# Optimization experiments

Hardware: AMD Instinct MI355X
Metric: run time of the kernel (lower is better)

## Reference

```python
import jax, jax.numpy as jnp
import numpy as np


def _sobel_kernels():
    # Three 3x3x3 stencils, one per axis: plane at index 0 = -1, plane at index 2 = +1
    # (the torch code also sets kernel[1,1,1]=0, which is already zero).
    ks = []
    for axis in range(3):
        k = np.zeros((3, 3, 3), np.float32)
        sl = [slice(None)] * 3
        sl[axis] = 0
        k[tuple(sl)] = -1.0
        sl[axis] = 2
        k[tuple(sl)] = 1.0
        ks.append(k)
    return np.stack(ks)  # [3, 3, 3, 3]


def setup_inputs() -> dict:
    key = jax.random.key(0)
    x = jax.random.normal(key, (2, 2, 160, 160, 160), dtype=jnp.float32)
    return {"x": x}


def reference(x):
    B, C, D, H, W = x.shape
    # replicate padding (torch F.pad mode='replicate' == jnp 'edge')
    xp = jnp.pad(x, ((0, 0), (0, 0), (1, 1), (1, 1), (1, 1)), mode="edge")
    kernels = jnp.asarray(_sobel_kernels())  # [3,3,3,3]
    # One fused depthwise conv: for each input channel, 3 directional outputs.
    # Grouped conv with feature_group_count=C: output channels [c*3 + d].
    w = jnp.broadcast_to(kernels[None], (C, 3, 3, 3, 3)).reshape(C * 3, 1, 3, 3, 3)
    g = jax.lax.conv_general_dilated(
        xp, w, window_strides=(1, 1, 1), padding="VALID",
        dimension_numbers=("NCDHW", "OIDHW", "NCDHW"),
        feature_group_count=C,
    )  # [B, C*3, D, H, W]
    g = g.reshape(B, C, 3, D, H, W)
    mag = jnp.sqrt(jnp.sum(g * g, axis=2))  # [B, C, D, H, W]
    # torch code cats per-(b,c) [1,1,D,H,W] slices along dim=1 -> [1, B*C, D, H, W]
    return mag.reshape(1, B * C, D, H, W)
```

## Files before the change

kernel.cpp:

```cpp
#include <hip/hip_runtime.h>
#include <math.h>

#define BCn 4
#define Dn 160
#define Hn 160
#define Wn 160
#define HWn (Hn * Wn)
#define W4q (Wn / 4)
#define COLS (Hn * W4q)
#define DCHUNK 5
#define NZC (Dn / DCHUNK)
#define XBLK (COLS / 256)
#define NWR (NZC * BCn)
#define BLOCK 256

typedef float f32x4 __attribute__((ext_vector_type(4)));

struct Plane {
  float4 Rs, Rd, Cs;
};

__device__ __forceinline__ Plane load_plane(const float* __restrict__ xb, int zz,
                                            int rm, int r0, int rp, int w4,
                                            bool ql, bool qr, bool fixL, bool fixR) {
  const int zc = zz < 0 ? 0 : (zz > Dn - 1 ? Dn - 1 : zz);
  const float* p = xb + (size_t)zc * HWn;

  const float4 vm = *(const float4*)(p + rm + w4);
  const float4 v0 = *(const float4*)(p + r0 + w4);
  const float4 vp = *(const float4*)(p + rp + w4);

  float lA = __shfl_up(vm.w, 1);
  float lB = __shfl_up(v0.w, 1);
  float lC = __shfl_up(vp.w, 1);
  float rA = __shfl_down(vm.x, 1);
  float rB = __shfl_down(v0.x, 1);
  float rC = __shfl_down(vp.x, 1);

  if (fixL) {
    lA = p[rm + w4 - 1];
    lB = p[r0 + w4 - 1];
    lC = p[rp + w4 - 1];
  }
  if (fixR) {
    rA = p[rm + w4 + 4];
    rB = p[r0 + w4 + 4];
    rC = p[rp + w4 + 4];
  }

  const float m0 = ql ? vm.x : lA;
  const float c0 = ql ? v0.x : lB;
  const float q0 = ql ? vp.x : lC;
  const float m5 = qr ? vm.w : rA;
  const float c5 = qr ? v0.w : rB;
  const float q5 = qr ? vp.w : rC;

  const float s0 = m0 + c0 + q0;
  const float s1 = vm.x + v0.x + vp.x;
  const float s2 = vm.y + v0.y + vp.y;
  const float s3 = vm.z + v0.z + vp.z;
  const float s4 = vm.w + v0.w + vp.w;
  const float s5 = m5 + c5 + q5;
  const float d0 = q0 - m0;
  const float d1 = vp.x - vm.x;
  const float d2 = vp.y - vm.y;
  const float d3 = vp.z - vm.z;
  const float d4 = vp.w - vm.w;
  const float d5 = q5 - m5;

  Plane out;
  const float t12 = s1 + s2, t23 = s2 + s3, t34 = s3 + s4;
  out.Rs.x = s0 + t12;
  out.Rs.y = t12 + s3;
  out.Rs.z = t23 + s4;
  out.Rs.w = t34 + s5;
  const float u12 = d1 + d2, u23 = d2 + d3, u34 = d3 + d4;
  out.Rd.x = d0 + u12;
  out.Rd.y = u12 + d3;
  out.Rd.z = u23 + d4;
  out.Rd.w = u34 + d5;
  out.Cs.x = s2 - s0;
  out.Cs.y = s3 - s1;
  out.Cs.z = s4 - s2;
  out.Cs.w = s5 - s3;
  return out;
}

__device__ __forceinline__ f32x4 mag4(const Plane& P0, const Plane& P1,
                                      const Plane& P2) {
  const float gdx = P2.Rs.x - P0.Rs.x;
  const float gdy = P2.Rs.y - P0.Rs.y;
  const float gdz = P2.Rs.z - P0.Rs.z;
  const float gdw = P2.Rs.w - P0.Rs.w;
  const float ghx = P0.Rd.x + P1.Rd.x + P2.Rd.x;
  const float ghy = P0.Rd.y + P1.Rd.y + P2.Rd.y;
  const float ghz = P0.Rd.z + P1.Rd.z + P2.Rd.z;
  const float ghw = P0.Rd.w + P1.Rd.w + P2.Rd.w;
  const float gwx = P0.Cs.x + P1.Cs.x + P2.Cs.x;
  const float gwy = P0.Cs.y + P1.Cs.y + P2.Cs.y;
  const float gwz = P0.Cs.z + P1.Cs.z + P2.Cs.z;
  const float gww = P0.Cs.w + P1.Cs.w + P2.Cs.w;
  f32x4 g;
  g.x = __builtin_amdgcn_sqrtf(fmaf(gdx, gdx, fmaf(ghx, ghx, gwx * gwx)));
  g.y = __builtin_amdgcn_sqrtf(fmaf(gdy, gdy, fmaf(ghy, ghy, gwy * gwy)));
  g.z = __builtin_amdgcn_sqrtf(fmaf(gdz, gdz, fmaf(ghz, ghz, gwz * gwz)));
  g.w = __builtin_amdgcn_sqrtf(fmaf(gdw, gdw, fmaf(ghw, ghw, gww * gww)));
  return g;
}

__global__ __launch_bounds__(BLOCK) void sobel3d_mag_kernel(
    const float* __restrict__ x, float* __restrict__ out) {
  const int F = blockIdx.x;
  const int k = F & 7;
  const int j = F >> 3;
  const int bx = j % XBLK;
  const int wr = (j / XBLK) * 8 + k;
  const int zc_idx = wr & (NZC - 1);
  const int bc = wr >> 5;

  const int col4 = bx * BLOCK + threadIdx.x;
  const int h = col4 / W4q;
  const int q = col4 - h * W4q;
  const int w4 = q * 4;
  const int d0 = zc_idx * DCHUNK;

  const float* xb = x + (size_t)bc * Dn * HWn;
  float* ob = out + (size_t)bc * Dn * HWn;

  const int hm = (h > 0) ? h - 1 : 0;
  const int hp = (h < Hn - 1) ? h + 1 : Hn - 1;
  const int rm = hm * Wn;
  const int r0 = h * Wn;
  const int rp = hp * Wn;

  const int lane = threadIdx.x & 63;
  const bool ql = (q == 0);
  const bool qr = (q == W4q - 1);
  const bool fixL = (lane == 0) && !ql;
  const bool fixR = (lane == 63) && !qr;

  Plane P0 = load_plane(xb, d0 - 1, rm, r0, rp, w4, ql, qr, fixL, fixR);
  Plane P1 = load_plane(xb, d0, rm, r0, rp, w4, ql, qr, fixL, fixR);

#pragma unroll
  for (int i = 0; i < DCHUNK; ++i) {
    const int z = d0 + i;
    Plane P2 = load_plane(xb, z + 1, rm, r0, rp, w4, ql, qr, fixL, fixR);
    __builtin_nontemporal_store(mag4(P0, P1, P2),
                                (f32x4*)(ob + (size_t)z * HWn + r0 + w4));
    P0 = P1;
    P1 = P2;
  }
}

extern "C" void kernel_launch(void* const* d_in, const int* in_sizes, int n_in,
                              void* d_out, int out_size, void* d_ws, size_t ws_size,
                              hipStream_t stream) {
  const float* x = (const float*)d_in[0];
  float* out = (float*)d_out;

  dim3 block(BLOCK);
  dim3 grid(XBLK * NZC * BCn);
  sobel3d_mag_kernel<<<grid, block, 0, stream>>>(x, out);
}
```

Measured before the change: 29.31 us.

## Stage each depth plane with row halo in LDS instead of three global row loads

Each block now cooperatively loads its 256 float4 columns plus a 41-column halo on each side of every z-plane into a double-buffered shared-memory array. Each thread then reads its row above, centre row and row below from LDS, replacing three separate global loads. The lane-0 and lane-63 neighbour fixups also come from LDS. The aim is to cut redundant global and L1 traffic on a kernel that is close to memory-bound. The cost is a __syncthreads per plane, extra LDS traffic, and extra halo loads of about 1.3x per plane.

```diff
diff --git a/kernel.cpp b/kernel.cpp
--- a/kernel.cpp
+++ b/kernel.cpp
@@ -11,80 +11,15 @@
 #define DCHUNK 5
 #define NZC (Dn / DCHUNK)
 #define XBLK (COLS / 256)
-#define NWR (NZC * BCn)
 #define BLOCK 256
+#define HALO 41
+#define STG (BLOCK + 2 * HALO)
 
 typedef float f32x4 __attribute__((ext_vector_type(4)));
 
 struct Plane {
   float4 Rs, Rd, Cs;
 };
-
-__device__ __forceinline__ Plane load_plane(const float* __restrict__ xb, int zz,
-                                            int rm, int r0, int rp, int w4,
-                                            bool ql, bool qr, bool fixL, bool fixR) {
-  const int zc = zz < 0 ? 0 : (zz > Dn - 1 ? Dn - 1 : zz);
-  const float* p = xb + (size_t)zc * HWn;
-
-  const float4 vm = *(const float4*)(p + rm + w4);
-  const float4 v0 = *(const float4*)(p + r0 + w4);
-  const float4 vp = *(const float4*)(p + rp + w4);
-
-  float lA = __shfl_up(vm.w, 1);
-  float lB = __shfl_up(v0.w, 1);
-  float lC = __shfl_up(vp.w, 1);
-  float rA = __shfl_down(vm.x, 1);
-  float rB = __shfl_down(v0.x, 1);
-  float rC = __shfl_down(vp.x, 1);
-
-  if (fixL) {
-    lA = p[rm + w4 - 1];
-    lB = p[r0 + w4 - 1];
-    lC = p[rp + w4 - 1];
-  }
-  if (fixR) {
-    rA = p[rm + w4 + 4];
-    rB = p[r0 + w4 + 4];
-    rC = p[rp + w4 + 4];
-  }
-
-  const float m0 = ql ? vm.x : lA;
-  const float c0 = ql ? v0.x : lB;
-  const float q0 = ql ? vp.x : lC;
-  const float m5 = qr ? vm.w : rA;
-  const float c5 = qr ? v0.w : rB;
-  const float q5 = qr ? vp.w : rC;
-
-  const float s0 = m0 + c0 + q0;
-  const float s1 = vm.x + v0.x + vp.x;
-  const float s2 = vm.y + v0.y + vp.y;
-  const float s3 = vm.z + v0.z + vp.z;
-  const float s4 = vm.w + v0.w + vp.w;
-  const float s5 = m5 + c5 + q5;
-  const float d0 = q0 - m0;
-  const float d1 = vp.x - vm.x;
-  const float d2 = vp.y - vm.y;
-  const float d3 = vp.z - vm.z;
-  const float d4 = vp.w - vm.w;
-  const float d5 = q5 - m5;
-
-  Plane out;
-  const float t12 = s1 + s2, t23 = s2 + s3, t34 = s3 + s4;
-  out.Rs.x = s0 + t12;
-  out.Rs.y = t12 + s3;
-  out.Rs.z = t23 + s4;
-  out.Rs.w = t34 + s5;
-  const float u12 = d1 + d2, u23 = d2 + d3, u34 = d3 + d4;
-  out.Rd.x = d0 + u12;
-  out.Rd.y = u12 + d3;
-  out.Rd.z = u23 + d4;
-  out.Rd.w = u34 + d5;
-  out.Cs.x = s2 - s0;
-  out.Cs.y = s3 - s1;
-  out.Cs.z = s4 - s2;
-  out.Cs.w = s5 - s3;
-  return out;
-}
 
 __device__ __forceinline__ f32x4 mag4(const Plane& P0, const Plane& P1,
                                       const Plane& P2) {
@@ -110,6 +45,8 @@
 
 __global__ __launch_bounds__(BLOCK) void sobel3d_mag_kernel(
     const float* __restrict__ x, float* __restrict__ out) {
+  __shared__ float4 buf[2][STG];
+
   const int F = blockIdx.x;
   const int k = F & 7;
   const int j = F >> 3;
@@ -118,7 +55,9 @@
   const int zc_idx = wr & (NZC - 1);
   const int bc = wr >> 5;
 
-  const int col4 = bx * BLOCK + threadIdx.x;
+  const int tid = threadIdx.x;
+  const int base = bx * BLOCK;
+  const int col4 = base + tid;
   const int h = col4 / W4q;
   const int q = col4 - h * W4q;
   const int w4 = q * 4;
@@ -127,25 +66,105 @@
   const float* xb = x + (size_t)bc * Dn * HWn;
   float* ob = out + (size_t)bc * Dn * HWn;
 
-  const int hm = (h > 0) ? h - 1 : 0;
-  const int hp = (h < Hn - 1) ? h + 1 : Hn - 1;
-  const int rm = hm * Wn;
-  const int r0 = h * Wn;
-  const int rp = hp * Wn;
+  int g0 = base - HALO + tid;
+  int c0 = g0 < 0 ? g0 + W4q : (g0 >= COLS ? g0 - W4q : g0);
+  c0 = c0 < 0 ? 0 : (c0 > COLS - 1 ? COLS - 1 : c0);
+  int g1 = g0 + BLOCK;
+  int c1 = g1 >= COLS ? g1 - W4q : g1;
+  c1 = c1 > COLS - 1 ? COLS - 1 : c1;
+  const bool extra = tid < (STG - BLOCK);
 
-  const int lane = threadIdx.x & 63;
+  const int s = tid + HALO;
+  const int lane = tid & 63;
   const bool ql = (q == 0);
   const bool qr = (q == W4q - 1);
-  const bool fixL = (lane == 0) && !ql;
-  const bool fixR = (lane == 63) && !qr;
 
-  Plane P0 = load_plane(xb, d0 - 1, rm, r0, rp, w4, ql, qr, fixL, fixR);
-  Plane P1 = load_plane(xb, d0, rm, r0, rp, w4, ql, qr, fixL, fixR);
+  auto stage = [&](int b, int zz) {
+    const int zc = zz < 0 ? 0 : (zz > Dn - 1 ? Dn - 1 : zz);
+    const float* p = xb + (size_t)zc * HWn;
+    const float4 v0 = *(const float4*)(p + c0 * 4);
+    buf[b][tid] = v0;
+    if (extra) {
+      const float4 v1 = *(const float4*)(p + c1 * 4);
+      buf[b][tid + BLOCK] = v1;
+    }
+  };
+
+  auto rdplane = [&](int b) -> Plane {
+    const float4 vm = buf[b][s - W4q];
+    const float4 v0 = buf[b][s];
+    const float4 vp = buf[b][s + W4q];
+
+    float lA = __shfl_up(vm.w, 1);
+    float lB = __shfl_up(v0.w, 1);
+    float lC = __shfl_up(vp.w, 1);
+    float rA = __shfl_down(vm.x, 1);
+    float rB = __shfl_down(v0.x, 1);
+    float rC = __shfl_down(vp.x, 1);
+    if (lane == 0) {
+      lA = buf[b][s - W4q - 1].w;
+      lB = buf[b][s - 1].w;
+      lC = buf[b][s + W4q - 1].w;
+    }
+    if (lane == 63) {
+      rA = buf[b][s - W4q + 1].x;
+      rB = buf[b][s + 1].x;
+      rC = buf[b][s + W4q + 1].x;
+    }
+
+    const float m0 = ql ? vm.x : lA;
+    const float c0v = ql ? v0.x : lB;
+    const float q0v = ql ? vp.x : lC;
+    const float m5 = qr ? vm.w : rA;
+    const float c5 = qr ? v0.w : rB;
+    const float q5 = qr ? vp.w : rC;
+
+    const float s0 = m0 + c0v + q0v;
+    const float s1 = vm.x + v0.x + vp.x;
+    const float s2 = vm.y + v0.y + vp.y;
+    const float s3 = vm.z + v0.z + vp.z;
+    const float s4 = vm.w + v0.w + vp.w;
+    const float s5 = m5 + c5 + q5;
+    const float d0v = q0v - m0;
+    const float d1 = vp.x - vm.x;
+    const float d2 = vp.y - vm.y;
+    const float d3 = vp.z - vm.z;
+    const float d4 = vp.w - vm.w;
+    const float d5 = q5 - m5;
+
+    Plane o;
+    const float t12 = s1 + s2, t23 = s2 + s3, t34 = s3 + s4;
+    o.Rs.x = s0 + t12;
+    o.Rs.y = t12 + s3;
+    o.Rs.z = t23 + s4;
+    o.Rs.w = t34 + s5;
+    const float u12 = d1 + d2, u23 = d2 + d3, u34 = d3 + d4;
+    o.Rd.x = d0v + u12;
+    o.Rd.y = u12 + d3;
+    o.Rd.z = u23 + d4;
+    o.Rd.w = u34 + d5;
+    o.Cs.x = s2 - s0;
+    o.Cs.y = s3 - s1;
+    o.Cs.z = s4 - s2;
+    o.Cs.w = s5 - s3;
+    return o;
+  };
+
+  const int r0 = h * Wn;
+
+  stage(0, d0 - 1);
+  stage(1, d0);
+  __syncthreads();
+  Plane P0 = rdplane(0);
+  Plane P1 = rdplane(1);
+  __syncthreads();
 
 #pragma unroll
   for (int i = 0; i < DCHUNK; ++i) {
     const int z = d0 + i;
-    Plane P2 = load_plane(xb, z + 1, rm, r0, rp, w4, ql, qr, fixL, fixR);
+    stage(i & 1, z + 1);
+    __syncthreads();
+    Plane P2 = rdplane(i & 1);
     __builtin_nontemporal_store(mag4(P0, P1, P2),
                                 (f32x4*)(ob + (size_t)z * HWn + r0 + w4));
     P0 = P1;
```

Result: slower. 30.76 us (+4.9%).
